# Optimization experiments

Measured on AMD Instinct MI355X. Metric: run time of the kernel, lower is better.

## Reference

```python
import jax, jax.numpy as jnp
import numpy as np

B, T, D, A = 64, 1024, 768, 128

def setup_inputs() -> dict:
    key = jax.random.key(0)
    k1, k2, k3 = jax.random.split(key, 3)
    x = jax.random.normal(k1, (B, T, D), dtype=jnp.float32)
    # glorot_normal-style scaling for the learned projections
    W1 = jax.random.normal(k2, (D, A), dtype=jnp.float32) * np.sqrt(2.0 / (D + A))
    W2 = jax.random.normal(k3, (A, T), dtype=jnp.float32) * np.sqrt(2.0 / (A + T))
    return {"x": x, "W1": W1, "W2": W2}

def reference(x, W1, W2):
    # x: [B, T, D], W1: [D, A], W2: [A, T]
    OA = jnp.tanh(jnp.einsum('btd,da->bta', x, W1))      # [B, T, A]
    OA = jnp.einsum('bta,as->bts', OA, W2)               # [B, T, T]
    OA = jax.nn.softmax(OA, axis=-2)                     # softmax over source-time axis
    # ot[b,s,d] = sum_t x[b,t,d] * OA[b,t,s]  (x^T @ OA, then transpose back)
    ot = jnp.einsum('btd,bts->bsd', x, OA)               # [B, T, D]
    return ot
```

## Files before the change

### kernel.cpp

```cpp
#include <hip/hip_runtime.h>
#include <math.h>

#define B_ 64
#define T_ 1024
#define D_ 768
#define A_ 128

typedef __attribute__((ext_vector_type(4))) float f32x4;
typedef __attribute__((ext_vector_type(8))) short s16x8;
typedef __attribute__((ext_vector_type(4))) short s16x4;

__device__ inline short f2b(float f) {
  union { float f; unsigned u; } v; v.f = f;
  unsigned r = (v.u + 0x7FFFu + ((v.u >> 16) & 1u)) >> 16;
  return (short)r;
}
__device__ inline float b2f(short s) {
  union { unsigned u; float f; } v; v.u = ((unsigned)(unsigned short)s) << 16;
  return v.f;
}

__device__ inline void gll16(const void* g, const void* lds) {
  __builtin_amdgcn_global_load_lds(
      (const __attribute__((address_space(1))) unsigned*)g,
      (__attribute__((address_space(3))) unsigned*)lds, 16, 0, 0);
}

__global__ __launch_bounds__(512, 2)
void g4_div(const short* __restrict__ Ag, const short* __restrict__ Bg,
            const float* __restrict__ Rs, float* __restrict__ Cg) {
  __shared__ __align__(16) short AS[2][16384];
  __shared__ __align__(16) short BS[2][16384];
  unsigned nwg = gridDim.x;
  unsigned L = blockIdx.x;
  unsigned xcd = L & 7u, base = L >> 3;
  unsigned q = nwg >> 3, r = nwg & 7u;
  unsigned id = (xcd < r ? xcd * (q + 1) : r * (q + 1) + (xcd - r) * q) + base;
  const int bz = id / 12;
  const int rem = id - bz * 12;
  const int by = rem / 3, bx = rem - (rem / 3) * 3;
  const int m0 = by * 256, n0 = bx * 256;

  const short* Ab = Ag + (size_t)bz * (T_ * T_);
  const short* Bb = Bg + (size_t)bz * (D_ * T_);
  const float* rsb = Rs + (size_t)bz * T_;
  float* Cb = Cg + (size_t)bz * (T_ * D_);

  const int tid = threadIdx.x;
  const int w = tid >> 6, lane = tid & 63;
  const int wr = w >> 2, wc = w & 3;
  const int lr = lane & 15, lq = lane >> 4;
  const int swzk = (lane & 7) ^ ((lane >> 3) & 7);
  const int abase = (wr * 128 + lr) * 64;
  const int bbase = (wc * 64 + lr) * 64;
  const int sx = lr & 7;
  const int sl0 = (lq ^ sx) * 8;
  const int sl1 = ((4 + lq) ^ sx) * 8;

  f32x4 acc[8][4] = {};
  s16x8 bq[4][2];

#define STG(dst, src, r0, kt)                                                  \
  { _Pragma("unroll")                                                          \
    for (int jj = 0; jj < 2; ++jj) {                                           \
      int rr = jj * 64 + w * 8 + (lane >> 3);                                  \
      gll16((src) + (size_t)((r0) + rr) * 1024 + (kt) + swzk * 8,              \
            (dst) + jj * 4096 + w * 512);                                      \
    } }

#define PH2(P, Q0, VM, ...)                                                    \
  {                                                                            \
    s16x8 a0_ = *(const s16x8*)&AS[P][abase + (2 * (Q0)) * 1024 + sl0];        \
    s16x8 a1_ = *(const s16x8*)&AS[P][abase + (2 * (Q0)) * 1024 + sl1];        \
    s16x8 a2_ = *(const s16x8*)&AS[P][abase + (2 * (Q0) + 1) * 1024 + sl0];    \
    s16x8 a3_ = *(const s16x8*)&AS[P][abase + (2 * (Q0) + 1) * 1024 + sl1];    \
    if ((Q0) == 0) {                                                           \
      _Pragma("unroll")                                                        \
      for (int nf = 0; nf < 4; ++nf) {                                         \
        bq[nf][0] = *(const s16x8*)&BS[P][bbase + nf * 1024 + sl0];            \
        bq[nf][1] = *(const s16x8*)&BS[P][bbase + nf * 1024 + sl1];            \
      }                                                                        \
    }                                                                          \
    __VA_ARGS__;                                                               \
    VM;                                                                        \
    __builtin_amdgcn_s_barrier();                                              \
    asm volatile("s_waitcnt lgkmcnt(0)" ::: "memory");                         \
    __builtin_amdgcn_s_setprio(1);                                             \
    _Pragma("unroll")                                                          \
    for (int nf = 0; nf < 4; ++nf) {                                           \
      acc[2*(Q0)][nf]   = __builtin_amdgcn_mfma_f32_16x16x32_bf16(a0_, bq[nf][0], acc[2*(Q0)][nf], 0, 0, 0);   \
      acc[2*(Q0)+1][nf] = __builtin_amdgcn_mfma_f32_16x16x32_bf16(a2_, bq[nf][0], acc[2*(Q0)+1][nf], 0, 0, 0); \
    }                                                                          \
    s16x8 a4_ = *(const s16x8*)&AS[P][abase + (2 * (Q0) + 2) * 1024 + sl0];    \
    s16x8 a5_ = *(const s16x8*)&AS[P][abase + (2 * (Q0) + 2) * 1024 + sl1];    \
    s16x8 a6_ = *(const s16x8*)&AS[P][abase + (2 * (Q0) + 3) * 1024 + sl0];    \
    s16x8 a7_ = *(const s16x8*)&AS[P][abase + (2 * (Q0) + 3) * 1024 + sl1];    \
    _Pragma("unroll")                                                          \
    for (int nf = 0; nf < 4; ++nf) {                                           \
      acc[2*(Q0)][nf]   = __builtin_amdgcn_mfma_f32_16x16x32_bf16(a1_, bq[nf][1], acc[2*(Q0)][nf], 0, 0, 0);   \
      acc[2*(Q0)+1][nf] = __builtin_amdgcn_mfma_f32_16x16x32_bf16(a3_, bq[nf][1], acc[2*(Q0)+1][nf], 0, 0, 0); \
    }                                                                          \
    _Pragma("unroll")                                                          \
    for (int nf = 0; nf < 4; ++nf) {                                           \
      acc[2*(Q0)+2][nf] = __builtin_amdgcn_mfma_f32_16x16x32_bf16(a4_, bq[nf][0], acc[2*(Q0)+2][nf], 0, 0, 0); \
      acc[2*(Q0)+3][nf] = __builtin_amdgcn_mfma_f32_16x16x32_bf16(a6_, bq[nf][0], acc[2*(Q0)+3][nf], 0, 0, 0); \
    }                                                                          \
    _Pragma("unroll")                                                          \
    for (int nf = 0; nf < 4; ++nf) {                                           \
      acc[2*(Q0)+2][nf] = __builtin_amdgcn_mfma_f32_16x16x32_bf16(a5_, bq[nf][1], acc[2*(Q0)+2][nf], 0, 0, 0); \
      acc[2*(Q0)+3][nf] = __builtin_amdgcn_mfma_f32_16x16x32_bf16(a7_, bq[nf][1], acc[2*(Q0)+3][nf], 0, 0, 0); \
    }                                                                          \
    __builtin_amdgcn_s_setprio(0);                                             \
    __builtin_amdgcn_s_barrier();                                              \
  }

#define VM4 asm volatile("s_waitcnt vmcnt(4)" ::: "memory")
#define VM0 asm volatile("s_waitcnt vmcnt(0)" ::: "memory")
#define NOP (void)0

  STG(&BS[0][0],    Bb, n0,       0);
  STG(&BS[0][8192], Bb, n0 + 128, 0);
  STG(&AS[0][0],    Ab, m0,       0);
  STG(&AS[0][8192], Ab, m0 + 128, 0);
  STG(&BS[1][0],    Bb, n0,       64);
  STG(&BS[1][8192], Bb, n0 + 128, 64);
  VM4;
  __builtin_amdgcn_s_barrier();

  for (int j = 0; j < 7; ++j) {
    const int kb = j * 128;
    PH2(0, 0, NOP,
        STG(&AS[1][0],    Ab, m0,       kb + 64);
        STG(&AS[1][8192], Ab, m0 + 128, kb + 64));
    PH2(0, 2, VM4,
        STG(&BS[0][0],    Bb, n0,       kb + 128);
        STG(&BS[0][8192], Bb, n0 + 128, kb + 128));
    PH2(1, 0, NOP,
        STG(&AS[0][0],    Ab, m0,       kb + 128);
        STG(&AS[0][8192], Ab, m0 + 128, kb + 128));
    PH2(1, 2, VM4,
        STG(&BS[1][0],    Bb, n0,       kb + 192);
        STG(&BS[1][8192], Bb, n0 + 128, kb + 192));
  }
  PH2(0, 0, NOP,
      STG(&AS[1][0],    Ab, m0,       960);
      STG(&AS[1][8192], Ab, m0 + 128, 960));
  PH2(0, 2, VM0, NOP);
  PH2(1, 0, NOP, NOP);
  PH2(1, 2, NOP, NOP);

#undef STG
#undef PH2
#undef VM4
#undef VM0
#undef NOP

#pragma unroll
  for (int mf = 0; mf < 8; ++mf) {
    f32x4 rsv = *(const f32x4*)&rsb[m0 + wr * 128 + mf * 16 + lq * 4];
    f32x4 inv;
#pragma unroll
    for (int qq = 0; qq < 4; ++qq) {
      float iv;
      asm("v_rcp_f32 %0, %1" : "=v"(iv) : "v"(rsv[qq]));
      inv[qq] = iv;
    }
#pragma unroll
    for (int nf = 0; nf < 4; ++nf) {
      int m = m0 + wr * 128 + mf * 16 + lq * 4;
      int n = n0 + wc * 64 + nf * 16 + lr;
#pragma unroll
      for (int qq = 0; qq < 4; ++qq)
        Cb[(size_t)(m + qq) * D_ + n] = acc[mf][nf][qq] * inv[qq];
    }
  }
}

template<int BK, bool BF32, bool TANH_, bool WT, bool OB16, bool EXPSUM, bool XT>
__global__ __launch_bounds__(256, 2)
void gemm_bt(const short* __restrict__ Ab, const void* __restrict__ Bv,
             void* __restrict__ Cv, float* __restrict__ Rs,
             short* __restrict__ Xt,
             int M, int N, int K,
             long sA, long sB, long sC, int gx, int gy) {
  constexpr int OPS = 128 * BK;
  constexpr int BOUNCE = 128 * 136;
  constexpr int BASE = (2 * OPS > BOUNCE ? 2 * OPS : BOUNCE);
  __shared__ __align__(16) short SMEM[BASE + (XT ? 64 * 136 : 0)];
  short* As = SMEM;
  short* Bs = SMEM + OPS;
  short* Ts = SMEM + 2 * OPS;

  unsigned nwg = gridDim.x;
  unsigned L = blockIdx.x;
  unsigned xcd = L & 7u, base = L >> 3;
  unsigned q = nwg >> 3, r = nwg & 7u;
  unsigned id = (xcd < r ? xcd * (q + 1) : r * (q + 1) + (xcd - r) * q) + base;
  const int gxy = gx * gy;
  const int bz = id / gxy;
  const int rem = id - bz * gxy;
  const int by = rem / gx;
  const int bx = rem - by * gx;

  const int tid = threadIdx.x;
  const int w = tid >> 6, lane = tid & 63;
  const int n0 = bx * 128, m0 = by * 128;
  const int wr = w >> 1, wc = w & 1;
  const int lr = lane & 15, lq = lane >> 4;
  const short* A = Ab + (size_t)sA * bz;
  const short* Bb16 = nullptr; const float* Bf32 = nullptr;
  if (BF32) Bf32 = (const float*)Bv + (size_t)sB * bz;
  else      Bb16 = (const short*)Bv + (size_t)sB * bz;
  short* Xtb = XT ? Xt + (size_t)bz * ((size_t)D_ * T_) : nullptr;

  f32x4 acc[4][4] = {};

  constexpr int LPR = BK / 8;
  constexpr int RPC = 64 / LPR;
  constexpr int CPT = BK / 16;
  const int rl = lane / LPR;
  const int cl = (lane % LPR) * 8;

  for (int k0 = 0; k0 < K; k0 += BK) {
    __syncthreads();
#pragma unroll
    for (int i = 0; i < CPT; ++i) {
      int chunk = w * CPT + i;
      int row = chunk * RPC + rl;
      gll16(A + (size_t)(m0 + row) * K + k0 + cl, As + chunk * 512);
    }
    s16x8 parr[4];
    if (!BF32) {
#pragma unroll
      for (int i = 0; i < CPT; ++i) {
        int chunk = w * CPT + i;
        int row = chunk * RPC + rl;
        gll16(Bb16 + (size_t)(n0 + row) * K + k0 + cl, Bs + chunk * 512);
      }
    } else {
#pragma unroll
      for (int u = 0; u < 4; ++u) {
        int c = tid * 4 + u;
        int row = c >> 3, k8 = c & 7;
        const float* gp = Bf32 + (size_t)(n0 + row) * K + k0 + k8 * 8;
        float4 f0 = *(const float4*)gp;
        float4 f1 = *(const float4*)(gp + 4);
        s16x8 p;
        p[0] = f2b(f0.x); p[1] = f2b(f0.y); p[2] = f2b(f0.z); p[3] = f2b(f0.w);
        p[4] = f2b(f1.x); p[5] = f2b(f1.y); p[6] = f2b(f1.z); p[7] = f2b(f1.w);
        parr[u] = p;
        *(s16x8*)&Bs[row * 64 + k8 * 8] = p;
      }
    }
    __syncthreads();
#pragma unroll
    for (int kk = 0; kk < BK / 32; ++kk) {
      s16x8 a[4], b[4];
#pragma unroll
      for (int mf = 0; mf < 4; ++mf)
        a[mf] = *(const s16x8*)&As[(wr * 64 + mf * 16 + lr) * BK + kk * 32 + lq * 8];
#pragma unroll
      for (int nf = 0; nf < 4; ++nf)
        b[nf] = *(const s16x8*)&Bs[(wc * 64 + nf * 16 + lr) * BK + kk * 32 + lq * 8];
#pragma unroll
      for (int mf = 0; mf < 4; ++mf)
#pragma unroll
        for (int nf = 0; nf < 4; ++nf)
          acc[mf][nf] = __builtin_amdgcn_mfma_f32_16x16x32_bf16(
              a[mf], b[nf], acc[mf][nf], 0, 0, 0);
    }
    if constexpr (XT) {
#pragma unroll
      for (int u = 0; u < 4; ++u) {
        int c = tid * 4 + u;
        int row = c >> 3, k8 = c & 7;
#pragma unroll
        for (int j = 0; j < 8; ++j) Ts[(k8 * 8 + j) * 136 + row] = parr[u][j];
      }
      __syncthreads();
#pragma unroll
      for (int u = 0; u < 4; ++u) {
        int task = tid + u * 256;
        int dd = task >> 4, t8 = task & 15;
        *(s16x8*)&Xtb[(size_t)(k0 + dd) * T_ + n0 + t8 * 8] =
            *(const s16x8*)&Ts[dd * 136 + t8 * 8];
      }
    }
  }

  if (WT && OB16) {
    __syncthreads();
    float psum[4] = {0.f, 0.f, 0.f, 0.f};
#pragma unroll
    for (int mf = 0; mf < 4; ++mf)
#pragma unroll
      for (int nf = 0; nf < 4; ++nf) {
        int ml = wr * 64 + mf * 16 + lq * 4;
        int nl = wc * 64 + nf * 16 + lr;
        s16x4 pk;
#pragma unroll
        for (int qq = 0; qq < 4; ++qq) {
          float v = acc[mf][nf][qq];
          if (TANH_) v = tanhf(v);
          if (EXPSUM) v = __expf(v);
          pk[qq] = f2b(v);
          if (EXPSUM) psum[nf] += b2f(pk[qq]);
        }
        *(s16x4*)&SMEM[nl * 136 + ml] = pk;
      }
    if (EXPSUM) {
      float* rs = Rs + (size_t)T_ * bz;
#pragma unroll
      for (int nf = 0; nf < 4; ++nf) {
        psum[nf] += __shfl_xor(psum[nf], 16);
        psum[nf] += __shfl_xor(psum[nf], 32);
      }
      if (lq == 0) {
#pragma unroll
        for (int nf = 0; nf < 4; ++nf)
          atomicAdd(&rs[n0 + wc * 64 + nf * 16 + lr], psum[nf]);
      }
    }
    __syncthreads();
    short* C = (short*)Cv + (size_t)sC * bz;
#pragma unroll
    for (int it = 0; it < 8; ++it) {
      int row = it * 16 + (tid >> 4);
      int col = (tid & 15) * 8;
      *(s16x8*)(C + (size_t)(n0 + row) * M + m0 + col) =
          *(const s16x8*)&SMEM[row * 136 + col];
    }
  } else if (WT) {
    float* C = (float*)Cv + (size_t)sC * bz;
#pragma unroll
    for (int mf = 0; mf < 4; ++mf)
#pragma unroll
      for (int nf = 0; nf < 4; ++nf) {
        int mbase = m0 + wr * 64 + mf * 16 + lq * 4;
        int n = n0 + wc * 64 + nf * 16 + lr;
#pragma unroll
        for (int qq = 0; qq < 4; ++qq) {
          float v = acc[mf][nf][qq];
          if (TANH_) v = tanhf(v);
          C[(size_t)n * M + mbase + qq] = v;
        }
      }
  } else {
    float* C = (float*)Cv + (size_t)sC * bz;
#pragma unroll
    for (int mf = 0; mf < 4; ++mf)
#pragma unroll
      for (int nf = 0; nf < 4; ++nf) {
        int m = m0 + wr * 64 + mf * 16 + lq * 4;
        int n = n0 + wc * 64 + nf * 16 + lr;
#pragma unroll
        for (int qq = 0; qq < 4; ++qq) {
          float v = acc[mf][nf][qq];
          if (TANH_) v = tanhf(v);
          C[(size_t)(m + qq) * N + n] = v;
        }
      }
  }
}

__global__ __launch_bounds__(256)
void transpose_cvt(const float* __restrict__ src, short* __restrict__ dst,
                   int R, int C) {
  __shared__ float sh[64][65];
  const int tid = threadIdx.x;
  const float* s = src + (size_t)blockIdx.z * R * C;
  short* d = dst + (size_t)blockIdx.z * R * C;
  const int r0 = blockIdx.y * 64, c0 = blockIdx.x * 64;
#pragma unroll
  for (int u = 0; u < 4; ++u) {
    int e = tid + u * 256;
    int rr = e >> 4, cc4 = (e & 15) * 4;
    float4 v = *(const float4*)&s[(size_t)(r0 + rr) * C + c0 + cc4];
    sh[rr][cc4 + 0] = v.x;
    sh[rr][cc4 + 1] = v.y;
    sh[rr][cc4 + 2] = v.z;
    sh[rr][cc4 + 3] = v.w;
  }
  __syncthreads();
#pragma unroll
  for (int u = 0; u < 4; ++u) {
    int e = tid + u * 256;
    int dr = e >> 4, tc4 = (e & 15) * 4;
    s16x4 pk;
#pragma unroll
    for (int j = 0; j < 4; ++j) pk[j] = f2b(sh[tc4 + j][dr]);
    *(s16x4*)&d[(size_t)(c0 + dr) * R + r0 + tc4] = pk;
  }
}

extern "C" void kernel_launch(void* const* d_in, const int* in_sizes, int n_in,
                              void* d_out, int out_size, void* d_ws, size_t ws_size,
                              hipStream_t stream) {
  const float* x  = (const float*)d_in[0];
  const float* W1 = (const float*)d_in[1];
  const float* W2 = (const float*)d_in[2];
  float* out = (float*)d_out;

  short* xt  = (short*)d_ws;
  short* W1t = xt + (size_t)B_ * D_ * T_;
  short* W2t = W1t + (size_t)A_ * D_;
  short* H   = W2t + (size_t)T_ * A_;
  float* rs  = (float*)(H + (size_t)B_ * T_ * A_);
  short* St  = (short*)(rs + (size_t)B_ * T_);
  size_t fixed_bytes = (size_t)((char*)St - (char*)xt);
  long avail = (long)ws_size - (long)fixed_bytes;
  long per_b = (long)T_ * T_ * sizeof(short);
  int chunk = (int)(avail > 0 ? avail / per_b : 0);
  if (chunk > B_) chunk = B_;
  if (chunk < 1) chunk = 1;

  hipMemsetAsync(rs, 0, (size_t)B_ * T_ * sizeof(float), stream);

  transpose_cvt<<<dim3(A_ / 64, D_ / 64, 1), 256, 0, stream>>>(W1, W1t, D_, A_);
  transpose_cvt<<<dim3(T_ / 64, A_ / 64, 1), 256, 0, stream>>>(W2, W2t, A_, T_);

  gemm_bt<64, true, true, true, true, false, true>
      <<<(T_ / 128) * (A_ / 128) * B_, 256, 0, stream>>>(
      W1t, x, H, nullptr, xt, A_, T_, D_, 0, (long)T_ * D_, (long)T_ * A_,
      T_ / 128, A_ / 128);

  for (int b0 = 0; b0 < B_; b0 += chunk) {
    int nb = B_ - b0; if (nb > chunk) nb = chunk;
    gemm_bt<128, false, false, true, true, true, false>
        <<<(T_ / 128) * (T_ / 128) * nb, 256, 0, stream>>>(
        H + (size_t)b0 * T_ * A_, W2t, St, rs + (size_t)b0 * T_, nullptr,
        T_, T_, A_, (long)T_ * A_, 0, (long)T_ * T_,
        T_ / 128, T_ / 128);
    g4_div<<<12 * nb, 512, 0, stream>>>(
        St, xt + (size_t)b0 * (size_t)D_ * T_, rs + (size_t)b0 * T_,
        out + (size_t)b0 * (size_t)T_ * D_);
  }
}
```

Before: 285.3 us.

## Fuse tanh projection GEMM with score GEMM and exp into one kernel

Measured after the change: 256.7 us. -10.0%, faster.

```diff
diff --git a/kernel.cpp b/kernel.cpp
--- a/kernel.cpp
+++ b/kernel.cpp
@@ -176,92 +176,70 @@
   }
 }
 
-template<int BK, bool BF32, bool TANH_, bool WT, bool OB16, bool EXPSUM, bool XT>
 __global__ __launch_bounds__(256, 2)
-void gemm_bt(const short* __restrict__ Ab, const void* __restrict__ Bv,
-             void* __restrict__ Cv, float* __restrict__ Rs,
-             short* __restrict__ Xt,
-             int M, int N, int K,
-             long sA, long sB, long sC, int gx, int gy) {
-  constexpr int OPS = 128 * BK;
-  constexpr int BOUNCE = 128 * 136;
-  constexpr int BASE = (2 * OPS > BOUNCE ? 2 * OPS : BOUNCE);
-  __shared__ __align__(16) short SMEM[BASE + (XT ? 64 * 136 : 0)];
+void g12(const short* __restrict__ W1tg, const float* __restrict__ xg,
+         const short* __restrict__ W2tg, short* __restrict__ Stg,
+         float* __restrict__ rsg, short* __restrict__ xtg, int nb) {
+  __shared__ __align__(16) short SMEM[33792];
   short* As = SMEM;
-  short* Bs = SMEM + OPS;
-  short* Ts = SMEM + 2 * OPS;
+  short* Bs = SMEM + 8192;
+  short* Ts = SMEM + 16384;
+  short* Hs = SMEM;
+  short* B2 = SMEM + 16384;
 
   unsigned nwg = gridDim.x;
   unsigned L = blockIdx.x;
   unsigned xcd = L & 7u, base = L >> 3;
   unsigned q = nwg >> 3, r = nwg & 7u;
   unsigned id = (xcd < r ? xcd * (q + 1) : r * (q + 1) + (xcd - r) * q) + base;
-  const int gxy = gx * gy;
-  const int bz = id / gxy;
-  const int rem = id - bz * gxy;
-  const int by = rem / gx;
-  const int bx = rem - by * gx;
+  const int bz = id >> 3, bt = id & 7;
+  const int t0 = bt * 128;
+
+  const float* xb = xg + (size_t)bz * T_ * D_;
+  short* Xtb = xtg + (size_t)bz * ((size_t)D_ * T_);
+  short* Stb = Stg + (size_t)bz * (T_ * T_);
+  float* rsb = rsg + (size_t)bz * T_;
 
   const int tid = threadIdx.x;
   const int w = tid >> 6, lane = tid & 63;
-  const int n0 = bx * 128, m0 = by * 128;
   const int wr = w >> 1, wc = w & 1;
   const int lr = lane & 15, lq = lane >> 4;
-  const short* A = Ab + (size_t)sA * bz;
-  const short* Bb16 = nullptr; const float* Bf32 = nullptr;
-  if (BF32) Bf32 = (const float*)Bv + (size_t)sB * bz;
-  else      Bb16 = (const short*)Bv + (size_t)sB * bz;
-  short* Xtb = XT ? Xt + (size_t)bz * ((size_t)D_ * T_) : nullptr;
+  const int r8 = lane >> 3, c8 = lane & 7;
 
   f32x4 acc[4][4] = {};
 
-  constexpr int LPR = BK / 8;
-  constexpr int RPC = 64 / LPR;
-  constexpr int CPT = BK / 16;
-  const int rl = lane / LPR;
-  const int cl = (lane % LPR) * 8;
-
-  for (int k0 = 0; k0 < K; k0 += BK) {
-    __syncthreads();
-#pragma unroll
-    for (int i = 0; i < CPT; ++i) {
-      int chunk = w * CPT + i;
-      int row = chunk * RPC + rl;
-      gll16(A + (size_t)(m0 + row) * K + k0 + cl, As + chunk * 512);
+  for (int k0 = 0; k0 < D_; k0 += 64) {
+    __syncthreads();
+#pragma unroll
+    for (int i = 0; i < 4; ++i) {
+      int chunk = w * 4 + i;
+      int row = chunk * 8 + r8;
+      gll16(W1tg + (size_t)row * D_ + k0 + c8 * 8, As + chunk * 512);
     }
     s16x8 parr[4];
-    if (!BF32) {
-#pragma unroll
-      for (int i = 0; i < CPT; ++i) {
-        int chunk = w * CPT + i;
-        int row = chunk * RPC + rl;
-        gll16(Bb16 + (size_t)(n0 + row) * K + k0 + cl, Bs + chunk * 512);
-      }
-    } else {
-#pragma unroll
-      for (int u = 0; u < 4; ++u) {
-        int c = tid * 4 + u;
-        int row = c >> 3, k8 = c & 7;
-        const float* gp = Bf32 + (size_t)(n0 + row) * K + k0 + k8 * 8;
-        float4 f0 = *(const float4*)gp;
-        float4 f1 = *(const float4*)(gp + 4);
-        s16x8 p;
-        p[0] = f2b(f0.x); p[1] = f2b(f0.y); p[2] = f2b(f0.z); p[3] = f2b(f0.w);
-        p[4] = f2b(f1.x); p[5] = f2b(f1.y); p[6] = f2b(f1.z); p[7] = f2b(f1.w);
-        parr[u] = p;
-        *(s16x8*)&Bs[row * 64 + k8 * 8] = p;
-      }
-    }
-    __syncthreads();
-#pragma unroll
-    for (int kk = 0; kk < BK / 32; ++kk) {
+#pragma unroll
+    for (int u = 0; u < 4; ++u) {
+      int c = tid * 4 + u;
+      int row = c >> 3, k8 = c & 7;
+      const float* gp = xb + (size_t)(t0 + row) * D_ + k0 + k8 * 8;
+      float4 f0 = *(const float4*)gp;
+      float4 f1 = *(const float4*)(gp + 4);
+      s16x8 p;
+      p[0] = f2b(f0.x); p[1] = f2b(f0.y); p[2] = f2b(f0.z); p[3] = f2b(f0.w);
+      p[4] = f2b(f1.x); p[5] = f2b(f1.y); p[6] = f2b(f1.z); p[7] = f2b(f1.w);
+      parr[u] = p;
+      *(s16x8*)&Bs[row * 64 + k8 * 8] = p;
+    }
+    __syncthreads();
+#pragma unroll
+    for (int kk = 0; kk < 2; ++kk) {
       s16x8 a[4], b[4];
 #pragma unroll
       for (int mf = 0; mf < 4; ++mf)
-        a[mf] = *(const s16x8*)&As[(wr * 64 + mf * 16 + lr) * BK + kk * 32 + lq * 8];
+        a[mf] = *(const s16x8*)&As[(wr * 64 + mf * 16 + lr) * 64 + kk * 32 + lq * 8];
 #pragma unroll
       for (int nf = 0; nf < 4; ++nf)
-        b[nf] = *(const s16x8*)&Bs[(wc * 64 + nf * 16 + lr) * BK + kk * 32 + lq * 8];
+        b[nf] = *(const s16x8*)&Bs[(wc * 64 + nf * 16 + lr) * 64 + kk * 32 + lq * 8];
 #pragma unroll
       for (int mf = 0; mf < 4; ++mf)
 #pragma unroll
@@ -269,26 +247,70 @@
           acc[mf][nf] = __builtin_amdgcn_mfma_f32_16x16x32_bf16(
               a[mf], b[nf], acc[mf][nf], 0, 0, 0);
     }
-    if constexpr (XT) {
-#pragma unroll
-      for (int u = 0; u < 4; ++u) {
-        int c = tid * 4 + u;
-        int row = c >> 3, k8 = c & 7;
-#pragma unroll
-        for (int j = 0; j < 8; ++j) Ts[(k8 * 8 + j) * 136 + row] = parr[u][j];
+#pragma unroll
+    for (int u = 0; u < 4; ++u) {
+      int c = tid * 4 + u;
+      int row = c >> 3, k8 = c & 7;
+#pragma unroll
+      for (int j = 0; j < 8; ++j) Ts[(k8 * 8 + j) * 136 + row] = parr[u][j];
+    }
+    __syncthreads();
+#pragma unroll
+    for (int u = 0; u < 4; ++u) {
+      int task = tid + u * 256;
+      int dd = task >> 4, t8 = task & 15;
+      *(s16x8*)&Xtb[(size_t)(k0 + dd) * T_ + t0 + t8 * 8] =
+          *(const s16x8*)&Ts[dd * 136 + t8 * 8];
+    }
+  }
+
+  __syncthreads();
+#pragma unroll
+  for (int mf = 0; mf < 4; ++mf)
+#pragma unroll
+    for (int nf = 0; nf < 4; ++nf) {
+      int ml = wr * 64 + mf * 16 + lq * 4;
+      int nl = wc * 64 + nf * 16 + lr;
+      s16x4 pk;
+#pragma unroll
+      for (int qq = 0; qq < 4; ++qq) pk[qq] = f2b(tanhf(acc[mf][nf][qq]));
+      int slot = (ml >> 3) ^ (nl & 7);
+      *(s16x4*)&Hs[nl * 128 + (slot << 3) + (ml & 7)] = pk;
+    }
+  __syncthreads();
+
+  const int sxl = lr & 7;
+  for (int si = 0; si < 8; ++si) {
+    const int s0 = si * 128;
+#pragma unroll
+    for (int u = 0; u < 8; ++u) {
+      int idx = tid + u * 256;
+      int row = idx >> 4, c16 = idx & 15;
+      *(s16x8*)&B2[row * 128 + ((c16 ^ (row & 7)) << 3)] =
+          *(const s16x8*)&W2tg[(size_t)(s0 + row) * A_ + c16 * 8];
+    }
+    __syncthreads();
+    f32x4 ac2[4][4] = {};
+#pragma unroll
+    for (int kk = 0; kk < 4; ++kk) {
+      s16x8 a[4], b[4];
+#pragma unroll
+      for (int mf = 0; mf < 4; ++mf) {
+        int row = wr * 64 + mf * 16 + lr;
+        a[mf] = *(const s16x8*)&Hs[row * 128 + (((kk * 4 + lq) ^ sxl) << 3)];
       }
-      __syncthreads();
-#pragma unroll
-      for (int u = 0; u < 4; ++u) {
-        int task = tid + u * 256;
-        int dd = task >> 4, t8 = task & 15;
-        *(s16x8*)&Xtb[(size_t)(k0 + dd) * T_ + n0 + t8 * 8] =
-            *(const s16x8*)&Ts[dd * 136 + t8 * 8];
+#pragma unroll
+      for (int nf = 0; nf < 4; ++nf) {
+        int row = wc * 64 + nf * 16 + lr;
+        b[nf] = *(const s16x8*)&B2[row * 128 + (((kk * 4 + lq) ^ sxl) << 3)];
       }
-    }
-  }
-
-  if (WT && OB16) {
+#pragma unroll
+      for (int mf = 0; mf < 4; ++mf)
+#pragma unroll
+        for (int nf = 0; nf < 4; ++nf)
+          ac2[mf][nf] = __builtin_amdgcn_mfma_f32_16x16x32_bf16(
+              a[mf], b[nf], ac2[mf][nf], 0, 0, 0);
+    }
     __syncthreads();
     float psum[4] = {0.f, 0.f, 0.f, 0.f};
 #pragma unroll
@@ -300,66 +322,31 @@
         s16x4 pk;
 #pragma unroll
         for (int qq = 0; qq < 4; ++qq) {
-          float v = acc[mf][nf][qq];
-          if (TANH_) v = tanhf(v);
-          if (EXPSUM) v = __expf(v);
+          float v = __expf(ac2[mf][nf][qq]);
           pk[qq] = f2b(v);
-          if (EXPSUM) psum[nf] += b2f(pk[qq]);
+          psum[nf] += b2f(pk[qq]);
         }
-        *(s16x4*)&SMEM[nl * 136 + ml] = pk;
+        *(s16x4*)&B2[nl * 136 + ml] = pk;
       }
-    if (EXPSUM) {
-      float* rs = Rs + (size_t)T_ * bz;
-#pragma unroll
-      for (int nf = 0; nf < 4; ++nf) {
-        psum[nf] += __shfl_xor(psum[nf], 16);
-        psum[nf] += __shfl_xor(psum[nf], 32);
-      }
-      if (lq == 0) {
-#pragma unroll
-        for (int nf = 0; nf < 4; ++nf)
-          atomicAdd(&rs[n0 + wc * 64 + nf * 16 + lr], psum[nf]);
-      }
-    }
-    __syncthreads();
-    short* C = (short*)Cv + (size_t)sC * bz;
+#pragma unroll
+    for (int nf = 0; nf < 4; ++nf) {
+      psum[nf] += __shfl_xor(psum[nf], 16);
+      psum[nf] += __shfl_xor(psum[nf], 32);
+    }
+    if (lq == 0) {
+#pragma unroll
+      for (int nf = 0; nf < 4; ++nf)
+        atomicAdd(&rsb[s0 + wc * 64 + nf * 16 + lr], psum[nf]);
+    }
+    __syncthreads();
 #pragma unroll
     for (int it = 0; it < 8; ++it) {
       int row = it * 16 + (tid >> 4);
       int col = (tid & 15) * 8;
-      *(s16x8*)(C + (size_t)(n0 + row) * M + m0 + col) =
-          *(const s16x8*)&SMEM[row * 136 + col];
-    }
-  } else if (WT) {
-    float* C = (float*)Cv + (size_t)sC * bz;
-#pragma unroll
-    for (int mf = 0; mf < 4; ++mf)
-#pragma unroll
-      for (int nf = 0; nf < 4; ++nf) {
-        int mbase = m0 + wr * 64 + mf * 16 + lq * 4;
-        int n = n0 + wc * 64 + nf * 16 + lr;
-#pragma unroll
-        for (int qq = 0; qq < 4; ++qq) {
-          float v = acc[mf][nf][qq];
-          if (TANH_) v = tanhf(v);
-          C[(size_t)n * M + mbase + qq] = v;
-        }
-      }
-  } else {
-    float* C = (float*)Cv + (size_t)sC * bz;
-#pragma unroll
-    for (int mf = 0; mf < 4; ++mf)
-#pragma unroll
-      for (int nf = 0; nf < 4; ++nf) {
-        int m = m0 + wr * 64 + mf * 16 + lq * 4;
-        int n = n0 + wc * 64 + nf * 16 + lr;
-#pragma unroll
-        for (int qq = 0; qq < 4; ++qq) {
-          float v = acc[mf][nf][qq];
-          if (TANH_) v = tanhf(v);
-          C[(size_t)(m + qq) * N + n] = v;
-        }
-      }
+      *(s16x8*)&Stb[(size_t)(s0 + row) * T_ + t0 + col] =
+          *(const s16x8*)&B2[row * 136 + col];
+    }
+    __syncthreads();
   }
 }
 
@@ -404,8 +391,7 @@
   short* xt  = (short*)d_ws;
   short* W1t = xt + (size_t)B_ * D_ * T_;
   short* W2t = W1t + (size_t)A_ * D_;
-  short* H   = W2t + (size_t)T_ * A_;
-  float* rs  = (float*)(H + (size_t)B_ * T_ * A_);
+  float* rs  = (float*)(W2t + (size_t)T_ * A_);
   short* St  = (short*)(rs + (size_t)B_ * T_);
   size_t fixed_bytes = (size_t)((char*)St - (char*)xt);
   long avail = (long)ws_size - (long)fixed_bytes;
@@ -419,18 +405,11 @@
   transpose_cvt<<<dim3(A_ / 64, D_ / 64, 1), 256, 0, stream>>>(W1, W1t, D_, A_);
   transpose_cvt<<<dim3(T_ / 64, A_ / 64, 1), 256, 0, stream>>>(W2, W2t, A_, T_);
 
-  gemm_bt<64, true, true, true, true, false, true>
-      <<<(T_ / 128) * (A_ / 128) * B_, 256, 0, stream>>>(
-      W1t, x, H, nullptr, xt, A_, T_, D_, 0, (long)T_ * D_, (long)T_ * A_,
-      T_ / 128, A_ / 128);
-
   for (int b0 = 0; b0 < B_; b0 += chunk) {
     int nb = B_ - b0; if (nb > chunk) nb = chunk;
-    gemm_bt<128, false, false, true, true, true, false>
-        <<<(T_ / 128) * (T_ / 128) * nb, 256, 0, stream>>>(
-        H + (size_t)b0 * T_ * A_, W2t, St, rs + (size_t)b0 * T_, nullptr,
-        T_, T_, A_, (long)T_ * A_, 0, (long)T_ * T_,
-        T_ / 128, T_ / 128);
+    g12<<<8 * nb, 256, 0, stream>>>(
+        W1t, x + (size_t)b0 * T_ * D_, W2t, St,
+        rs + (size_t)b0 * T_, xt + (size_t)b0 * (size_t)D_ * T_, nb);
     g4_div<<<12 * nb, 512, 0, stream>>>(
         St, xt + (size_t)b0 * (size_t)D_ * T_, rs + (size_t)b0 * T_,
         out + (size_t)b0 * (size_t)T_ * D_);
```
